# Optimization experiments

Hardware: AMD Instinct MI355X
Metric: run time of the kernel (lower is better)

Reference implementation:

```python
import jax, jax.numpy as jnp
import numpy as np

IN, H, T = 1024, 2048, 2048

def setup_inputs() -> dict:
    key = jax.random.key(0)
    ks = jax.random.split(key, 10)
    x = jax.random.normal(ks[0], (1, T, IN), dtype=jnp.float32)
    # strictly increasing timestamps
    time = jnp.cumsum(jax.random.uniform(ks[1], (T,), dtype=jnp.float32))
    # xavier-ish scaled weights, uniform(0,1) biases as in init_weights
    W_ih = jax.random.normal(ks[2], (4 * H, IN), dtype=jnp.float32) * (1.0 / np.sqrt(IN))
    W_hh = jax.random.normal(ks[3], (4 * H, H), dtype=jnp.float32) * (1.0 / np.sqrt(H))
    b_ih = jax.random.uniform(ks[4], (4 * H,), dtype=jnp.float32)
    b_hh = jax.random.uniform(ks[5], (4 * H,), dtype=jnp.float32)
    decay_w = jax.random.normal(ks[6], (H,), dtype=jnp.float32)
    decay_b = jax.random.uniform(ks[7], (H,), dtype=jnp.float32)
    h0 = jax.random.normal(ks[8], (1, H), dtype=jnp.float32) * 0.1
    c0 = jax.random.normal(ks[9], (1, H), dtype=jnp.float32) * 0.1
    return {"x": x, "time": time, "W_ih": W_ih, "W_hh": W_hh, "b_ih": b_ih,
            "b_hh": b_hh, "decay_w": decay_w, "decay_b": decay_b, "h0": h0, "c0": c0}


def reference(x, time, W_ih, W_hh, b_ih, b_hh, decay_w, decay_b, h0, c0):
    Tn = x.shape[1]
    Hn = h0.shape[1]
    # dt[i] = time[i] - time[i-1], dt[0] = 0
    dt = jnp.concatenate([jnp.zeros((1,), x.dtype), time[1:] - time[:-1]])
    # step i (i>0) decays h with gamma(dt[i-1]); step 0 uses gamma = 1
    dt_prev = jnp.concatenate([jnp.zeros((1,), x.dtype), dt[:-1]])  # [T]
    gamma = jnp.exp(-jax.nn.relu(dt_prev[:, None] * decay_w[None, :] + decay_b[None, :]))  # [T,H]
    gamma = jnp.where((jnp.arange(Tn) > 0)[:, None], gamma, jnp.ones((), x.dtype))
    # precompute input contribution for all steps: [T, 4H]
    xg = x[0] @ W_ih.T + b_ih + b_hh

    def step(carry, inp):
        h, c = carry  # [H], [H]
        xg_t, gamma_t = inp
        h = h * gamma_t
        gates = xg_t + h @ W_hh.T  # [4H]
        i_, f_, g_, o_ = jnp.split(gates, 4)
        i_ = jax.nn.sigmoid(i_)
        f_ = jax.nn.sigmoid(f_)
        g_ = jnp.tanh(g_)
        o_ = jax.nn.sigmoid(o_)
        c = f_ * c + i_ * g_
        h = o_ * jnp.tanh(c)
        return (h, c), h

    (h_f, c_f), hs = jax.lax.scan(step, (h0[0], c0[0]), (xg, gamma))  # hs: [T,H]
    # dot-product attention pooling against final hidden state
    attn = hs @ h_f  # [T]
    w = jax.nn.softmax(attn)
    context = w @ hs  # [H]
    return context[None, :]  # [1, H]
```

## Files before the change

### kernel.cpp

```cpp
#include <hip/hip_runtime.h>
#include <hip/hip_bf16.h>

#define H 2048
#define T 2048
#define INPUT 1024
#define FOURH 8192
#define NBLK 256
#define RING 512

typedef __attribute__((ext_vector_type(8))) short bf16x8;
typedef __attribute__((ext_vector_type(4))) float f32x4_t;

__device__ __forceinline__ unsigned short f2bf(float f) {
  union { float f; unsigned u; } v; v.f = f;
  unsigned r = v.u + 0x7FFFu + ((v.u >> 16) & 1u);
  return (unsigned short)(r >> 16);
}

__device__ __forceinline__ float fast_tanh(float x) {
  float e = __expf(fminf(-2.f * x, 80.f));
  return (1.f - e) / (1.f + e);
}

__global__ void prep_kernel(const float* __restrict__ x, const float* __restrict__ W_ih,
                            const float* __restrict__ time_, short* __restrict__ xb,
                            short* __restrict__ wb, float* __restrict__ dtp,
                            unsigned* __restrict__ flags) {
  size_t i = (size_t)blockIdx.x * blockDim.x + threadIdx.x;
  size_t stride = (size_t)gridDim.x * blockDim.x;
  if (i < (size_t)T * INPUT) xb[i] = (short)f2bf(x[i]);
  for (size_t j = i; j < (size_t)FOURH * INPUT; j += stride) wb[j] = (short)f2bf(W_ih[j]);
  if (i < T) dtp[i] = (i >= 2) ? (time_[i - 1] - time_[i - 2]) : 0.0f;
  if (i < NBLK) flags[i] = 0u;
}

__global__ void __launch_bounds__(256)
gemm_xg(const short* __restrict__ A, const short* __restrict__ B,
        const float* __restrict__ b_ih, const float* __restrict__ b_hh,
        float* __restrict__ xg) {
  int wave = threadIdx.x >> 6;
  int lane = threadIdx.x & 63;
  int bid = blockIdx.x;
  int m0 = (bid & 127) << 4;
  int n0 = ((bid >> 7) << 6) + (wave << 4);
  int r16 = lane & 15, q = lane >> 4;
  const short* ap = A + (size_t)(m0 + r16) * INPUT + q * 8;
  const short* bp = B + (size_t)(n0 + r16) * INPUT + q * 8;
  f32x4_t acc = {0.f, 0.f, 0.f, 0.f};
#pragma unroll 4
  for (int k = 0; k < INPUT; k += 32) {
    bf16x8 av = *(const bf16x8*)(ap + k);
    bf16x8 bv = *(const bf16x8*)(bp + k);
    acc = __builtin_amdgcn_mfma_f32_16x16x32_bf16(av, bv, acc, 0, 0, 0);
  }
  int n = n0 + r16;
  float bias = b_ih[n] + b_hh[n];
#pragma unroll
  for (int r = 0; r < 4; ++r) {
    int m = m0 + q * 4 + r;
    xg[(size_t)m * FOURH + n] = acc[r] + bias;
  }
}

__device__ __forceinline__ void epoch_bar(unsigned* flags, unsigned e) {
  __syncthreads();
  if (threadIdx.x == 0)
    __hip_atomic_store(&flags[blockIdx.x], e, __ATOMIC_RELEASE, __HIP_MEMORY_SCOPE_AGENT);
  if (threadIdx.x < NBLK) {
    while (__hip_atomic_load(&flags[threadIdx.x], __ATOMIC_RELAXED,
                             __HIP_MEMORY_SCOPE_AGENT) < e) {
    }
  }
  __builtin_amdgcn_fence(__ATOMIC_ACQUIRE, "agent");
  __syncthreads();
}

__global__ void __launch_bounds__(512, 2)
lstm_rec(const float* __restrict__ xg, const float* __restrict__ W_hh,
         const float* __restrict__ decay_w, const float* __restrict__ decay_b,
         const float* __restrict__ h0, const float* __restrict__ c0,
         const float* __restrict__ dtp, float* __restrict__ hs,
         unsigned long long* ring, unsigned* flags) {
  const int wave = threadIdx.x >> 6;
  const int lane = threadIdx.x & 63;
  const int u = (blockIdx.x << 3) + wave;
  __shared__ __align__(16) float lh[H];

  float wreg[4][32];
#pragma unroll
  for (int g = 0; g < 4; ++g) {
    const float* wr = W_hh + (size_t)(g * H + u) * H + (lane << 2);
#pragma unroll
    for (int p = 0; p < 8; ++p)
      *(f32x4_t*)&wreg[g][p << 2] = *(const f32x4_t*)(wr + (p << 8));
  }
  const float dw = decay_w[u], db = decay_b[u];
  float c = c0[u];
  if (lane == 0) {
    union { float f; unsigned u; } hv; hv.f = h0[u];
    __hip_atomic_store(&ring[u], (1ull << 32) | hv.u, __ATOMIC_RELAXED,
                       __HIP_MEMORY_SCOPE_AGENT);
  }

  for (int t = 0; t < T; ++t) {
    if ((t & 255) == 0 && t) epoch_bar(flags, (unsigned)(t >> 8));

    float xv = 0.f, gam = 0.f;
    if (lane < 4) xv = xg[(size_t)t * FOURH + (size_t)lane * H + u];
    if (lane == 0 && t + 1 < T) gam = __expf(-fmaxf(0.f, dtp[t + 1] * dw + db));

    const unsigned want = (unsigned)t + 1u;
    unsigned long long* sp =
        ring + (((size_t)(t & (RING - 1)) << 11) | (unsigned)((wave << 8) + lane));
    unsigned long long w0, w1, w2, w3;
    for (;;) {
      w0 = __hip_atomic_load(sp,       __ATOMIC_RELAXED, __HIP_MEMORY_SCOPE_AGENT);
      w1 = __hip_atomic_load(sp + 64,  __ATOMIC_RELAXED, __HIP_MEMORY_SCOPE_AGENT);
      w2 = __hip_atomic_load(sp + 128, __ATOMIC_RELAXED, __HIP_MEMORY_SCOPE_AGENT);
      w3 = __hip_atomic_load(sp + 192, __ATOMIC_RELAXED, __HIP_MEMORY_SCOPE_AGENT);
      int bad = ((unsigned)(w0 >> 32) != want) | ((unsigned)(w1 >> 32) != want) |
                ((unsigned)(w2 >> 32) != want) | ((unsigned)(w3 >> 32) != want);
      if (!__any(bad)) break;
    }
    {
      float* lw = lh + (wave << 8) + lane;
      union { unsigned u; float f; } v;
      v.u = (unsigned)w0; lw[0]   = v.f;
      v.u = (unsigned)w1; lw[64]  = v.f;
      v.u = (unsigned)w2; lw[128] = v.f;
      v.u = (unsigned)w3; lw[192] = v.f;
    }
    __syncthreads();

    float a0 = 0.f, a1 = 0.f, a2 = 0.f, a3 = 0.f;
#pragma unroll
    for (int p = 0; p < 8; ++p) {
      f32x4_t h4 = *(const f32x4_t*)(lh + (p << 8) + (lane << 2));
#pragma unroll
      for (int e = 0; e < 4; ++e) {
        float h = h4[e];
        a0 += wreg[0][(p << 2) + e] * h;
        a1 += wreg[1][(p << 2) + e] * h;
        a2 += wreg[2][(p << 2) + e] * h;
        a3 += wreg[3][(p << 2) + e] * h;
      }
    }
#pragma unroll
    for (int s = 32; s >= 1; s >>= 1) {
      a0 += __shfl_xor(a0, s);
      a1 += __shfl_xor(a1, s);
      a2 += __shfl_xor(a2, s);
      a3 += __shfl_xor(a3, s);
    }

    {
      float pre = ((lane == 0) ? a0 : (lane == 1) ? a1 : (lane == 2) ? a2 : a3) + xv;
      float ps = (lane == 2) ? 2.f * pre : pre;
      float sg = 1.f / (1.f + __expf(-ps));
      float act = (lane == 2) ? 2.f * sg - 1.f : sg;
      float iv = __shfl(act, 0), fv = __shfl(act, 1), gv = __shfl(act, 2),
            ov = __shfl(act, 3);
      c = fv * c + iv * gv;
      float h = ov * fast_tanh(c);
      if (lane == 0 && t + 1 < T) {
        union { float f; unsigned u; } hv; hv.f = h * gam;
        size_t slot = (size_t)((t + 1) & (RING - 1)) << 11;
        __hip_atomic_store(&ring[slot | (unsigned)u],
                           (((unsigned long long)(t + 2)) << 32) | hv.u,
                           __ATOMIC_RELAXED, __HIP_MEMORY_SCOPE_AGENT);
      }
      if (lane == 1) hs[(size_t)t * H + u] = h;
    }
    __syncthreads();
  }
}

__global__ void attn_k(const float* __restrict__ hs, float* __restrict__ attn) {
  int t = blockIdx.x;
  const float* row = hs + (size_t)t * H;
  const float* hf = hs + (size_t)(T - 1) * H;
  float s = 0.f;
  for (int i = threadIdx.x; i < H; i += 256) s += row[i] * hf[i];
#pragma unroll
  for (int o = 32; o; o >>= 1) s += __shfl_down(s, o);
  __shared__ float wsum[4];
  if ((threadIdx.x & 63) == 0) wsum[threadIdx.x >> 6] = s;
  __syncthreads();
  if (threadIdx.x == 0) attn[t] = wsum[0] + wsum[1] + wsum[2] + wsum[3];
}

__global__ void softmax_k(float* __restrict__ a) {
  int tid = threadIdx.x;
  __shared__ float red[16];
  __shared__ float bcast;
  float m = -1e30f;
  for (int i = tid; i < T; i += 1024) m = fmaxf(m, a[i]);
#pragma unroll
  for (int o = 32; o; o >>= 1) m = fmaxf(m, __shfl_xor(m, o));
  if ((tid & 63) == 0) red[tid >> 6] = m;
  __syncthreads();
  if (tid == 0) {
    float mm = red[0];
    for (int i = 1; i < 16; ++i) mm = fmaxf(mm, red[i]);
    bcast = mm;
  }
  __syncthreads();
  float M = bcast, s = 0.f;
  for (int i = tid; i < T; i += 1024) { float e = __expf(a[i] - M); a[i] = e; s += e; }
#pragma unroll
  for (int o = 32; o; o >>= 1) s += __shfl_xor(s, o);
  if ((tid & 63) == 0) red[tid >> 6] = s;
  __syncthreads();
  if (tid == 0) {
    float ss = 0.f;
    for (int i = 0; i < 16; ++i) ss += red[i];
    bcast = 1.f / ss;
  }
  __syncthreads();
  float inv = bcast;
  for (int i = tid; i < T; i += 1024) a[i] *= inv;
}

__global__ void ctx_k(const float* __restrict__ hs, const float* __restrict__ w,
                      float* __restrict__ out) {
  int h = (blockIdx.x << 8) + threadIdx.x;
  int t0 = blockIdx.y << 6;
  float acc = 0.f;
  for (int t = t0; t < t0 + 64; ++t) acc += w[t] * hs[(size_t)t * H + h];
  atomicAdd(&out[h], acc);
}

extern "C" void kernel_launch(void* const* d_in, const int* in_sizes, int n_in,
                              void* d_out, int out_size, void* d_ws, size_t ws_size,
                              hipStream_t stream) {
  const float* x       = (const float*)d_in[0];
  const float* time_   = (const float*)d_in[1];
  const float* W_ih    = (const float*)d_in[2];
  const float* W_hh    = (const float*)d_in[3];
  const float* b_ih    = (const float*)d_in[4];
  const float* b_hh    = (const float*)d_in[5];
  const float* decay_w = (const float*)d_in[6];
  const float* decay_b = (const float*)d_in[7];
  const float* h0      = (const float*)d_in[8];
  const float* c0      = (const float*)d_in[9];

  char* ws = (char*)d_ws;
  float*    xg   = (float*)ws;
  float*    hs   = (float*)(ws + (64u << 20));
  short*    xb   = (short*)(ws + (80u << 20));
  short*    wb   = (short*)(ws + (84u << 20));
  unsigned long long* ring = (unsigned long long*)(ws + (100u << 20));
  float*    dtp  = (float*)(ws + (108u << 20));
  float*    attn = dtp + T;
  unsigned* flags = (unsigned*)(attn + T);

  prep_kernel<<<8192, 256, 0, stream>>>(x, W_ih, time_, xb, wb, dtp, flags);

  gemm_xg<<<16384, 256, 0, stream>>>(xb, wb, b_ih, b_hh, xg);

  {
    void* args[] = {&xg, (void*)&W_hh, (void*)&decay_w, (void*)&decay_b,
                    (void*)&h0, (void*)&c0, &dtp, &hs, &ring, &flags};
    (void)hipLaunchCooperativeKernel((void*)lstm_rec, dim3(NBLK), dim3(512), args, 0, stream);
  }

  attn_k<<<T, 256, 0, stream>>>(hs, attn);
  softmax_k<<<1, 1024, 0, stream>>>(attn);
  (void)hipMemsetAsync(d_out, 0, out_size * sizeof(float), stream);
  ctx_k<<<dim3(H / 256, T / 64), 256, 0, stream>>>(hs, attn, (float*)d_out);
}
```

Before: 6.428 ms.

## Relay recurrent hidden state through per-XCD mirror to cut cross-die polling

Picks one relay block per XCD, using the hardware XCC id and an atomic claim. That block polls the global ring for each step's hidden state and copies it into a per-XCD double-buffered mirror with per-wave flags. The other blocks on the same XCD spin briefly on the local flag and read the mirror with sc0 loads, so they should hit the shared L2 instead of polling the agent-scope ring across dies. If the flag does not arrive within a bounded number of tries, they fall back to the original ring polling. This adds an extra hop of latency on the relay path and relies on cache-coherence assumptions about sc0 loads within an XCD.

Result: slower. 10.55 ms (+64.1%).

```diff
diff --git a/kernel.cpp b/kernel.cpp
--- a/kernel.cpp
+++ b/kernel.cpp
@@ -25,13 +25,16 @@
 __global__ void prep_kernel(const float* __restrict__ x, const float* __restrict__ W_ih,
                             const float* __restrict__ time_, short* __restrict__ xb,
                             short* __restrict__ wb, float* __restrict__ dtp,
-                            unsigned* __restrict__ flags) {
+                            unsigned* __restrict__ flags, unsigned* __restrict__ mflag,
+                            unsigned* __restrict__ relay_slot) {
   size_t i = (size_t)blockIdx.x * blockDim.x + threadIdx.x;
   size_t stride = (size_t)gridDim.x * blockDim.x;
   if (i < (size_t)T * INPUT) xb[i] = (short)f2bf(x[i]);
   for (size_t j = i; j < (size_t)FOURH * INPUT; j += stride) wb[j] = (short)f2bf(W_ih[j]);
   if (i < T) dtp[i] = (i >= 2) ? (time_[i - 1] - time_[i - 2]) : 0.0f;
   if (i < NBLK) flags[i] = 0u;
+  if (i < 4096) mflag[i] = 0u;
+  if (i < 8) relay_slot[i] = 0xFFFFFFFFu;
 }
 
 __global__ void __launch_bounds__(256)
@@ -80,11 +83,22 @@
          const float* __restrict__ decay_w, const float* __restrict__ decay_b,
          const float* __restrict__ h0, const float* __restrict__ c0,
          const float* __restrict__ dtp, float* __restrict__ hs,
-         unsigned long long* ring, unsigned* flags) {
+         unsigned long long* ring, unsigned* flags, float* mirF,
+         unsigned* mflag, unsigned* relay_slot) {
   const int wave = threadIdx.x >> 6;
   const int lane = threadIdx.x & 63;
   const int u = (blockIdx.x << 3) + wave;
   __shared__ __align__(16) float lh[H];
+  __shared__ int s_xcd, s_isrelay;
+
+  if (threadIdx.x == 0) {
+    unsigned xcc;
+    asm volatile("s_getreg_b32 %0, hwreg(HW_REG_XCC_ID)" : "=s"(xcc));
+    xcc &= 7u;
+    s_xcd = (int)xcc;
+    unsigned old = atomicCAS(&relay_slot[xcc], 0xFFFFFFFFu, (unsigned)blockIdx.x);
+    s_isrelay = (old == 0xFFFFFFFFu) ? 1 : 0;
+  }
 
   float wreg[4][32];
 #pragma unroll
@@ -101,6 +115,9 @@
     __hip_atomic_store(&ring[u], (1ull << 32) | hv.u, __ATOMIC_RELAXED,
                        __HIP_MEMORY_SCOPE_AGENT);
   }
+  __syncthreads();
+  const int myxcd = s_xcd;
+  const bool isrelay = (s_isrelay != 0);
 
   for (int t = 0; t < T; ++t) {
     if ((t & 255) == 0 && t) epoch_bar(flags, (unsigned)(t >> 8));
@@ -110,25 +127,67 @@
     if (lane == 0 && t + 1 < T) gam = __expf(-fmaxf(0.f, dtp[t + 1] * dw + db));
 
     const unsigned want = (unsigned)t + 1u;
-    unsigned long long* sp =
-        ring + (((size_t)(t & (RING - 1)) << 11) | (unsigned)((wave << 8) + lane));
-    unsigned long long w0, w1, w2, w3;
-    for (;;) {
-      w0 = __hip_atomic_load(sp,       __ATOMIC_RELAXED, __HIP_MEMORY_SCOPE_AGENT);
-      w1 = __hip_atomic_load(sp + 64,  __ATOMIC_RELAXED, __HIP_MEMORY_SCOPE_AGENT);
-      w2 = __hip_atomic_load(sp + 128, __ATOMIC_RELAXED, __HIP_MEMORY_SCOPE_AGENT);
-      w3 = __hip_atomic_load(sp + 192, __ATOMIC_RELAXED, __HIP_MEMORY_SCOPE_AGENT);
-      int bad = ((unsigned)(w0 >> 32) != want) | ((unsigned)(w1 >> 32) != want) |
-                ((unsigned)(w2 >> 32) != want) | ((unsigned)(w3 >> 32) != want);
-      if (!__any(bad)) break;
-    }
-    {
+    if (isrelay) {
+      unsigned long long* sp =
+          ring + (((size_t)(t & (RING - 1)) << 11) | (unsigned)((wave << 8) + lane));
+      unsigned long long w0, w1, w2, w3;
+      for (;;) {
+        w0 = __hip_atomic_load(sp,       __ATOMIC_RELAXED, __HIP_MEMORY_SCOPE_AGENT);
+        w1 = __hip_atomic_load(sp + 64,  __ATOMIC_RELAXED, __HIP_MEMORY_SCOPE_AGENT);
+        w2 = __hip_atomic_load(sp + 128, __ATOMIC_RELAXED, __HIP_MEMORY_SCOPE_AGENT);
+        w3 = __hip_atomic_load(sp + 192, __ATOMIC_RELAXED, __HIP_MEMORY_SCOPE_AGENT);
+        int bad = ((unsigned)(w0 >> 32) != want) | ((unsigned)(w1 >> 32) != want) |
+                  ((unsigned)(w2 >> 32) != want) | ((unsigned)(w3 >> 32) != want);
+        if (!__any(bad)) break;
+      }
+      union { unsigned u; float f; } e0, e1, e2, e3;
+      e0.u = (unsigned)w0; e1.u = (unsigned)w1; e2.u = (unsigned)w2; e3.u = (unsigned)w3;
+      float* mp = mirF + (((size_t)myxcd << 12) |
+                          (unsigned)(((t & 1) << 11) | (wave << 8) | lane));
+      mp[0] = e0.f; mp[64] = e1.f; mp[128] = e2.f; mp[192] = e3.f;
+      asm volatile("s_waitcnt vmcnt(0)" ::: "memory");
+      if (lane == 0) {
+        volatile unsigned* fgp = mflag + ((myxcd << 9) | (wave << 6));
+        *fgp = want;
+      }
       float* lw = lh + (wave << 8) + lane;
-      union { unsigned u; float f; } v;
-      v.u = (unsigned)w0; lw[0]   = v.f;
-      v.u = (unsigned)w1; lw[64]  = v.f;
-      v.u = (unsigned)w2; lw[128] = v.f;
-      v.u = (unsigned)w3; lw[192] = v.f;
+      lw[0] = e0.f; lw[64] = e1.f; lw[128] = e2.f; lw[192] = e3.f;
+    } else {
+      const unsigned* fgp = mflag + ((myxcd << 9) | (wave << 6));
+      unsigned f = 0;
+#pragma unroll 1
+      for (int r = 0; r < 24; ++r) {
+        asm volatile("global_load_dword %0, %1, off sc0\n\ts_waitcnt vmcnt(0)"
+                     : "=v"(f) : "v"(fgp) : "memory");
+        if (f >= want) break;
+      }
+      if (f >= want) {
+        const float* mp = mirF + (((size_t)myxcd << 12) |
+                                  (unsigned)(((t & 1) << 11) | (wave << 8) | (lane << 2)));
+        f32x4_t h4;
+        asm volatile("global_load_dwordx4 %0, %1, off sc0\n\ts_waitcnt vmcnt(0)"
+                     : "=v"(h4) : "v"(mp) : "memory");
+        *(f32x4_t*)(lh + (wave << 8) + (lane << 2)) = h4;
+      } else {
+        unsigned long long* sp =
+            ring + (((size_t)(t & (RING - 1)) << 11) | (unsigned)((wave << 8) + lane));
+        unsigned long long w0, w1, w2, w3;
+        for (;;) {
+          w0 = __hip_atomic_load(sp,       __ATOMIC_RELAXED, __HIP_MEMORY_SCOPE_AGENT);
+          w1 = __hip_atomic_load(sp + 64,  __ATOMIC_RELAXED, __HIP_MEMORY_SCOPE_AGENT);
+          w2 = __hip_atomic_load(sp + 128, __ATOMIC_RELAXED, __HIP_MEMORY_SCOPE_AGENT);
+          w3 = __hip_atomic_load(sp + 192, __ATOMIC_RELAXED, __HIP_MEMORY_SCOPE_AGENT);
+          int bad = ((unsigned)(w0 >> 32) != want) | ((unsigned)(w1 >> 32) != want) |
+                    ((unsigned)(w2 >> 32) != want) | ((unsigned)(w3 >> 32) != want);
+          if (!__any(bad)) break;
+        }
+        float* lw = lh + (wave << 8) + lane;
+        union { unsigned u; float f; } v;
+        v.u = (unsigned)w0; lw[0]   = v.f;
+        v.u = (unsigned)w1; lw[64]  = v.f;
+        v.u = (unsigned)w2; lw[128] = v.f;
+        v.u = (unsigned)w3; lw[192] = v.f;
+      }
     }
     __syncthreads();
 
@@ -253,14 +312,19 @@
   float*    dtp  = (float*)(ws + (108u << 20));
   float*    attn = dtp + T;
   unsigned* flags = (unsigned*)(attn + T);
-
-  prep_kernel<<<8192, 256, 0, stream>>>(x, W_ih, time_, xb, wb, dtp, flags);
+  float*    mirF = (float*)(ws + (108u << 20) + (32u << 10));
+  unsigned* mflag = (unsigned*)(ws + (108u << 20) + (160u << 10));
+  unsigned* relay_slot = (unsigned*)(ws + (108u << 20) + (176u << 10));
+
+  prep_kernel<<<8192, 256, 0, stream>>>(x, W_ih, time_, xb, wb, dtp, flags, mflag,
+                                        relay_slot);
 
   gemm_xg<<<16384, 256, 0, stream>>>(xb, wb, b_ih, b_hh, xg);
 
   {
     void* args[] = {&xg, (void*)&W_hh, (void*)&decay_w, (void*)&decay_b,
-                    (void*)&h0, (void*)&c0, &dtp, &hs, &ring, &flags};
+                    (void*)&h0, (void*)&c0, &dtp, &hs, &ring, &flags,
+                    &mirF, &mflag, &relay_slot};
     (void)hipLaunchCooperativeKernel((void*)lstm_rec, dim3(NBLK), dim3(512), args, 0, stream);
   }
 
```
